# Performance work log

Hardware: AMD Instinct MI355X
Metric: run time of the kernel (lower is better)

Reference implementation:

```python
import jax, jax.numpy as jnp
import numpy as np

DIM = 1024
HEADS = 16
DHEAD = 64
MAXLEN = 512
B = 8
N = 256   # sequence (x) length
M = 256   # memory (h) length; M + N <= MAXLEN
INNER = HEADS * DHEAD


def setup_inputs() -> dict:
    key = jax.random.key(0)
    ks = jax.random.split(key, 8)
    w = lambda k, shape: jax.random.normal(k, shape, jnp.float32) * 0.02
    return {
        "x": jax.random.normal(ks[0], (B, N, DIM), jnp.float32),
        "h": jax.random.normal(ks[1], (B, M, DIM), jnp.float32),
        "Wqkv": w(ks[2], (DIM, 3 * INNER)),
        "Wkr": w(ks[3], (DIM, INNER)),
        "R": jax.random.normal(ks[4], (2 * MAXLEN, DIM), jnp.float32),
        "u": jax.random.normal(ks[5], (DHEAD,), jnp.float32),
        "v": jax.random.normal(ks[6], (DHEAD,), jnp.float32),
        "Wout": w(ks[7], (INNER, DIM)),
        "max_len": MAXLEN,
    }


def reference(x, h, Wqkv, Wkr, R, u, v, Wout, max_len):
    b, n, dim = x.shape
    m = h.shape[1]
    t = m + n
    scale = DHEAD ** -0.5

    cat = jnp.concatenate([h, x], axis=1)                     # [b, t, dim]
    qkv = cat @ Wqkv                                          # [b, t, 3*inner]
    q, k, val = [s.reshape(b, t, HEADS, DHEAD).transpose(0, 2, 1, 3)
                 for s in jnp.split(qkv, 3, axis=-1)]          # [b, h, t, d]

    # shifts[i, j] = (j - i) mod 2L, sliced as in the torch buffer
    ar = jnp.arange(2 * max_len)
    shifts_full = (ar[None, :] - ar[:, None]) % (2 * max_len)
    shifts = shifts_full[:max_len, :max_len][m:m + n, :t]      # [n, t]

    kr = (R @ Wkr)[shifts]                                    # gather: [n, t, inner]
    kr = kr.reshape(n, t, HEADS, DHEAD).transpose(2, 0, 1, 3)  # [h, n, t, d]

    q = q[:, :, m:]                                           # [b, h, n, d]

    term_a = jnp.einsum('bhnd,bhmd->bhnm', q, k)
    term_b = jnp.einsum('bhnd,hnmd->bhnm', q, kr)
    term_c = jnp.einsum('d,bhmd->bhm', u, k)[:, :, None, :]    # broadcast over n
    term_d = jnp.einsum('d,hnmd->hnm', v, kr)[None]            # broadcast over b
    dots = (term_a + term_b + term_c + term_d) * scale         # [b, h, n, t]

    qi = jnp.arange(n)[:, None]
    jm = jnp.arange(m)[None, :]
    js = jnp.arange(n)[None, :]
    mem_mask = jnp.where(qi > jm, -jnp.inf, 0.0)               # [n, m]
    ar_mask = jnp.where(js > qi, -jnp.inf, 0.0)                # [n, n]
    bias = jnp.concatenate([mem_mask, ar_mask], axis=1)[None, None]  # [1,1,n,t]

    attn = jax.nn.softmax(dots + bias, axis=-1)
    out = jnp.einsum('bhnm,bhmd->bhnd', attn, val)             # [b, h, n, d]
    out = out.transpose(0, 2, 1, 3).reshape(b, n, INNER)
    return out @ Wout
```

## Files before the change

### kernel.cpp

```cpp
#include <hip/hip_runtime.h>
#include <hip/hip_bf16.h>
#include <math.h>

typedef unsigned short u16;
typedef short bf16x8 __attribute__((ext_vector_type(8)));
typedef float f32x4 __attribute__((ext_vector_type(4)));

__device__ __forceinline__ u16 f2b(float f) {
    __hip_bfloat16 h = __float2bfloat16(f);
    return *reinterpret_cast<u16*>(&h);
}
__device__ __forceinline__ float b2f(u16 v) {
    __hip_bfloat16 h;
    *reinterpret_cast<u16*>(&h) = v;
    return __bfloat162float(h);
}

__device__ __forceinline__ void gload_lds16(const void* g, void* l) {
    __builtin_amdgcn_global_load_lds(
        (const __attribute__((address_space(1))) void*)g,
        (__attribute__((address_space(3))) void*)l, 16, 0, 0);
}


struct EpiQKV4 {
    u16 *Q, *Kt, *Vt;
    __device__ void operator()(int rowp, int colp, f32x4 vals) const {
        int b = colp >> 9, pos = colp & 511;
        int sec = rowp >> 10, cc = rowp & 1023;
        int head = cc >> 6, d0 = cc & 63;
        if (sec == 0) {
            if (pos < 256) return;
            ushort4 o;
            o.x = f2b(vals[0] * 0.125f); o.y = f2b(vals[1] * 0.125f);
            o.z = f2b(vals[2] * 0.125f); o.w = f2b(vals[3] * 0.125f);
            *(ushort4*)(Q + (long)((head * 8 + b) * 256 + (pos - 256)) * 64 + d0) = o;
        } else if (sec == 1) {
            ushort4 o;
            o.x = f2b(vals[0]); o.y = f2b(vals[1]);
            o.z = f2b(vals[2]); o.w = f2b(vals[3]);
            *(ushort4*)(Kt + (long)((b * 16 + head) * 512 + pos) * 64 + d0) = o;
        } else {
            #pragma unroll
            for (int r = 0; r < 4; ++r)
                Vt[(long)((b * 16 + head) * 64 + d0 + r) * 512 + pos] = f2b(vals[r]);
        }
    }
};

struct EpiStoreBf {
    u16* C; long ldc; long strideZ;
    __device__ void operator()(int z, int row, int col, float val) const {
        C[(long)z * strideZ + (long)row * ldc + col] = f2b(val);
    }
};


template <typename Epi, bool AF32, bool ROWMAP>
__device__ __forceinline__ void gemm_bt_body(char* smem, int bx, int by, int bz,
                                             const void* __restrict__ Av, int lda, long strideAz,
                                             const u16* __restrict__ B, int ldb, long strideBz,
                                             int K, Epi epi) {
    constexpr int LDT = 56;
    u16* As = (u16*)smem;
    u16* Bs = As + 64 * LDT;
    int n0 = bx * 64, m0 = by * 64, z = bz;
    const u16* Bb = B + (long)z * strideBz + (long)n0 * ldb;
    int tid = threadIdx.x;
    int wave = tid >> 6, lane = tid & 63;
    int wm = wave >> 1, wn = wave & 1;
    int lrow = lane & 15, lquad = lane >> 4;
    int srow = tid >> 2, scol = (tid & 3) * 8;
    f32x4 acc[2][2] = {};
    for (int k0 = 0; k0 < K; k0 += 32) {
        if constexpr (AF32) {
            long arow = m0 + srow;
            if constexpr (ROWMAP) arow = (arow < 256) ? 768 + arow : 0;
            const float* src = (const float*)Av + (long)z * strideAz + arow * lda + k0 + scol;
            float4 f0 = *(const float4*)src;
            float4 f1 = *(const float4*)(src + 4);
            bf16x8 vv;
            vv[0] = (short)f2b(f0.x); vv[1] = (short)f2b(f0.y);
            vv[2] = (short)f2b(f0.z); vv[3] = (short)f2b(f0.w);
            vv[4] = (short)f2b(f1.x); vv[5] = (short)f2b(f1.y);
            vv[6] = (short)f2b(f1.z); vv[7] = (short)f2b(f1.w);
            *(bf16x8*)(As + srow * LDT + scol) = vv;
        } else {
            const u16* Ab = (const u16*)Av + (long)z * strideAz + (long)m0 * lda;
            *(bf16x8*)(As + srow * LDT + scol) = *(const bf16x8*)(Ab + (long)srow * lda + k0 + scol);
        }
        *(bf16x8*)(Bs + srow * LDT + scol) = *(const bf16x8*)(Bb + (long)srow * ldb + k0 + scol);
        __syncthreads();
        bf16x8 af[2], bfr[2];
        #pragma unroll
        for (int mt = 0; mt < 2; ++mt)
            af[mt] = *(const bf16x8*)(As + (wm * 32 + mt * 16 + lrow) * LDT + lquad * 8);
        #pragma unroll
        for (int nt = 0; nt < 2; ++nt)
            bfr[nt] = *(const bf16x8*)(Bs + (wn * 32 + nt * 16 + lrow) * LDT + lquad * 8);
        #pragma unroll
        for (int mt = 0; mt < 2; ++mt)
            #pragma unroll
            for (int nt = 0; nt < 2; ++nt)
                acc[mt][nt] = __builtin_amdgcn_mfma_f32_16x16x32_bf16(af[mt], bfr[nt], acc[mt][nt], 0, 0, 0);
        __syncthreads();
    }
    #pragma unroll
    for (int mt = 0; mt < 2; ++mt)
        #pragma unroll
        for (int nt = 0; nt < 2; ++nt)
            #pragma unroll
            for (int r = 0; r < 4; ++r) {
                int row = m0 + wm * 32 + mt * 16 + lquad * 4 + r;
                int col = n0 + wn * 32 + nt * 16 + lrow;
                epi(z, row, col, acc[mt][nt][r]);
            }
}

__global__ __launch_bounds__(256) void prep_kernel(const float* __restrict__ x,
                                                   const float* __restrict__ h,
                                                   u16* __restrict__ catBF,
                                                   const float* __restrict__ Wqkv, u16* __restrict__ WqkvT,
                                                   const float* __restrict__ Wkr,  u16* __restrict__ WkrT,
                                                   const float* __restrict__ Wout, u16* __restrict__ WoutT,
                                                   u16* __restrict__ vtGuard) {
    __shared__ float tile[32][33];
    int bid = blockIdx.x, tid = threadIdx.x;
    if (bid == 7168) {
        ((unsigned int*)vtGuard)[tid] = 0u;
        return;
    }
    if (bid < 2048) {
        int idx = (bid * 256 + tid) * 8;
        int c = idx & 1023, r = idx >> 10;
        int b = r >> 9, pos = r & 511;
        const float* src = (pos < 256) ? h + ((long)(b * 256 + pos) * 1024 + c)
                                       : x + ((long)(b * 256 + pos - 256) * 1024 + c);
        float4 f0 = *(const float4*)src;
        float4 f1 = *(const float4*)(src + 4);
        bf16x8 vv;
        vv[0] = (short)f2b(f0.x); vv[1] = (short)f2b(f0.y);
        vv[2] = (short)f2b(f0.z); vv[3] = (short)f2b(f0.w);
        vv[4] = (short)f2b(f1.x); vv[5] = (short)f2b(f1.y);
        vv[6] = (short)f2b(f1.z); vv[7] = (short)f2b(f1.w);
        *(bf16x8*)(catBF + idx) = vv;
        return;
    }
    const float* W; u16* WT; int nb, kb; long ldw;
    if (bid < 5120) {
        int w = bid - 2048;
        W = Wqkv; WT = WqkvT; ldw = 3072;
        nb = (w % 96) * 32; kb = (w / 96) * 32;
    } else {
        int w = bid - 5120;
        if (w < 1024) { W = Wkr; WT = WkrT; }
        else          { W = Wout; WT = WoutT; w -= 1024; }
        ldw = 1024;
        nb = (w & 31) * 32; kb = (w >> 5) * 32;
    }
    {
        int lr = tid >> 3, lc = (tid & 7) * 4;
        float4 v = *(const float4*)&W[(long)(kb + lr) * ldw + nb + lc];
        tile[lr][lc + 0] = v.x; tile[lr][lc + 1] = v.y;
        tile[lr][lc + 2] = v.z; tile[lr][lc + 3] = v.w;
    }
    __syncthreads();
    int row = tid >> 3;
    int c4 = (tid & 7) * 4;
    ushort4 o;
    o.x = f2b(tile[c4 + 0][row]);
    o.y = f2b(tile[c4 + 1][row]);
    o.z = f2b(tile[c4 + 2][row]);
    o.w = f2b(tile[c4 + 3][row]);
    *(ushort4*)(WT + (long)(nb + row) * 1024 + kb + c4) = o;
}

__global__ __launch_bounds__(256, 3) void qkv_rwg_kernel(const u16* __restrict__ A, const u16* __restrict__ B,
                                                         EpiQKV4 eq,
                                                         const float* __restrict__ R, const u16* __restrict__ WkrT,
                                                         u16* __restrict__ RWg) {
    __shared__ alignas(16) char smem[49152];
    int bid0 = blockIdx.x;
    if (bid0 >= 640) {
        int bid2 = bid0 - 640;
        gemm_bt_body<EpiStoreBf, true, true>(smem, bid2 & 15, bid2 >> 4, 0,
            (const void*)R, 1024, 0L, WkrT, 1024, 0L, 1024, EpiStoreBf{RWg, 1024, 0});
        return;
    }
    int xcd = bid0 & 7, s = bid0 >> 3;
    int G = xcd * 10 + (s >> 3);
    int w = s & 7;
    int m0, n0;
    if (G < 64) {
        int nchunk = G >> 4, mrow = G & 15;
        m0 = 1024 + mrow * 128;
        n0 = (nchunk * 8 + w) * 128;
    } else {
        int G2 = G - 64;
        int nchunk = G2 >> 3, mrow = G2 & 7;
        m0 = mrow * 128;
        int c = nchunk * 8 + w;
        n0 = (c >> 1) * 512 + 256 + (c & 1) * 128;
    }
    int tid = threadIdx.x, wave = tid >> 6, lane = tid & 63;
    int wm = wave >> 1, wn = wave & 1;
    int lrow = lane & 15, lquad = lane >> 4;
    const u16* Ab = A + (long)m0 * 1024;
    const u16* Bb = B + (long)n0 * 1024;
    f32x4 acc[4][4] = {};

    int scperm = (((tid & 3) - ((tid >> 3) & 3)) & 3) * 8;
    int rsl = ((lquad + (lrow >> 1)) & 3) * 8;

    auto stage = [&](int buf, int k0) {
        u16* Asb = (u16*)smem + buf * 8192;
        u16* Bsb = Asb + 4096;
        int col = k0 + scperm;
        #pragma unroll
        for (int i = 0; i < 2; ++i) {
            int rowb = i * 64 + (tid >> 2);
            gload_lds16(Ab + (long)rowb * 1024 + col, Asb + i * 2048 + tid * 8);
            gload_lds16(Bb + (long)rowb * 1024 + col, Bsb + i * 2048 + tid * 8);
        }
    };
    auto compute = [&](int buf) {
        u16* Asb = (u16*)smem + buf * 8192;
        u16* Bsb = Asb + 4096;
        bf16x8 af[4], bfr[4];
        #pragma unroll
        for (int mt = 0; mt < 4; ++mt)
            af[mt] = *(const bf16x8*)(Asb + (wm * 64 + mt * 16 + lrow) * 32 + rsl);
        #pragma unroll
        for (int nt = 0; nt < 4; ++nt)
            bfr[nt] = *(const bf16x8*)(Bsb + (wn * 64 + nt * 16 + lrow) * 32 + rsl);
        __builtin_amdgcn_s_setprio(1);
        #pragma unroll
        for (int mt = 0; mt < 4; ++mt)
            #pragma unroll
            for (int nt = 0; nt < 4; ++nt)
                acc[mt][nt] = __builtin_amdgcn_mfma_f32_16x16x32_bf16(af[mt], bfr[nt], acc[mt][nt], 0, 0, 0);
        __builtin_amdgcn_s_setprio(0);
    };

    stage(0, 0);
    stage(1, 32);
    int cb = 0, sb = 2;
    for (int t = 0; t < 32; ++t) {
        if (t < 31) {
            asm volatile("s_waitcnt vmcnt(4)" ::: "memory");
        } else {
            asm volatile("s_waitcnt vmcnt(0)" ::: "memory");
        }
        __builtin_amdgcn_sched_barrier(0);
        __builtin_amdgcn_s_barrier();
        __builtin_amdgcn_sched_barrier(0);
        if (t < 30) stage(sb, (t + 2) * 32);
        __builtin_amdgcn_sched_barrier(0);
        compute(cb);
        cb = (cb == 2) ? 0 : cb + 1;
        sb = (sb == 2) ? 0 : sb + 1;
    }

    #pragma unroll
    for (int mt = 0; mt < 4; ++mt)
        #pragma unroll
        for (int nt = 0; nt < 4; ++nt) {
            int rowp = m0 + wm * 64 + mt * 16 + lquad * 4;
            int colp = n0 + wn * 64 + nt * 16 + lrow;
            eq(rowp, colp, acc[mt][nt]);
        }
}

__global__ __launch_bounds__(256, 4) void outproj_kernel(const u16* __restrict__ A,
                                                         const u16* __restrict__ B,
                                                         float* __restrict__ out) {
    __shared__ alignas(16) char smem[16384];
    int bid = blockIdx.x;
    int n0 = (bid & 15) * 64, m0 = (bid >> 4) * 64;
    int tid = threadIdx.x, wave = tid >> 6, lane = tid & 63;
    int wm = wave >> 1, wn = wave & 1;
    int lrow = lane & 15, lquad = lane >> 4;
    const u16* Ab = A + (long)m0 * 1024;
    const u16* Bb = B + (long)n0 * 1024;
    f32x4 acc[2][2] = {};

    int scperm = (((tid & 3) - ((tid >> 3) & 3)) & 3) * 8;
    int rsl = ((lquad + (lrow >> 1)) & 3) * 8;

    auto stage = [&](int buf, int k0) {
        u16* Asb = (u16*)smem + buf * 4096;
        u16* Bsb = Asb + 2048;
        int row = tid >> 2, col = k0 + scperm;
        gload_lds16(Ab + (long)row * 1024 + col, Asb + tid * 8);
        gload_lds16(Bb + (long)row * 1024 + col, Bsb + tid * 8);
    };
    auto compute = [&](int buf) {
        u16* Asb = (u16*)smem + buf * 4096;
        u16* Bsb = Asb + 2048;
        bf16x8 af[2], bfr[2];
        #pragma unroll
        for (int mt = 0; mt < 2; ++mt)
            af[mt] = *(const bf16x8*)(Asb + (wm * 32 + mt * 16 + lrow) * 32 + rsl);
        #pragma unroll
        for (int nt = 0; nt < 2; ++nt)
            bfr[nt] = *(const bf16x8*)(Bsb + (wn * 32 + nt * 16 + lrow) * 32 + rsl);
        #pragma unroll
        for (int mt = 0; mt < 2; ++mt)
            #pragma unroll
            for (int nt = 0; nt < 2; ++nt)
                acc[mt][nt] = __builtin_amdgcn_mfma_f32_16x16x32_bf16(af[mt], bfr[nt], acc[mt][nt], 0, 0, 0);
    };

    stage(0, 0);
    stage(1, 32);
    for (int t = 0; t < 31; ++t) {
        asm volatile("s_waitcnt vmcnt(2)" ::: "memory");
        __builtin_amdgcn_sched_barrier(0);
        __builtin_amdgcn_s_barrier();
        __builtin_amdgcn_sched_barrier(0);
        compute(t & 1);
        __builtin_amdgcn_sched_barrier(0);
        __builtin_amdgcn_s_barrier();
        __builtin_amdgcn_sched_barrier(0);
        if (t < 30) stage(t & 1, (t + 2) * 32);
    }
    asm volatile("s_waitcnt vmcnt(0)" ::: "memory");
    __builtin_amdgcn_sched_barrier(0);
    __builtin_amdgcn_s_barrier();
    __builtin_amdgcn_sched_barrier(0);
    compute(1);

    #pragma unroll
    for (int mt = 0; mt < 2; ++mt)
        #pragma unroll
        for (int nt = 0; nt < 2; ++nt)
            #pragma unroll
            for (int r = 0; r < 4; ++r)
                out[(long)(m0 + wm * 32 + mt * 16 + lquad * 4 + r) * 1024
                    + n0 + wn * 32 + nt * 16 + lrow] = acc[mt][nt][r];
}

__global__ __launch_bounds__(256, 4) void attn_kernel(const u16* __restrict__ Qs,
                                                      const u16* __restrict__ Kt,
                                                      const u16* __restrict__ VT,
                                                      const u16* __restrict__ RWg,
                                                      const float* __restrict__ uvec,
                                                      const float* __restrict__ vvec,
                                                      u16* __restrict__ attnOut) {
    constexpr int LDSW = 328;
    __shared__ alignas(16) u16 SQ[32 * LDSW];
    __shared__ float red[2][4][32];
    int id = blockIdx.x;
    int bh = id & 127, it = id >> 7;
    int b = bh >> 4, h = bh & 15;
    int i0 = it * 32;
    int w0 = i0;
    int tid = threadIdx.x, wave = tid >> 6, lane = tid & 63;
    int lrow = lane & 15, lquad = lane >> 4;

    bf16x8 aq[2][2], aqv[2][2];
    #pragma unroll
    for (int iu = 0; iu < 2; ++iu) {
        const u16* qbase = Qs + (long)((h * 8 + b) * 256 + i0 + iu * 16 + lrow) * 64;
        bf16x8 q0 = *(const bf16x8*)(qbase + lquad * 8);
        bf16x8 q1 = *(const bf16x8*)(qbase + 32 + lquad * 8);
        #pragma unroll
        for (int j = 0; j < 8; ++j) {
            float f0 = b2f((u16)q0[j]), f1 = b2f((u16)q1[j]);
            aq[iu][0][j]  = (short)f2b(f0 + 0.125f * uvec[lquad * 8 + j]);
            aq[iu][1][j]  = (short)f2b(f1 + 0.125f * uvec[32 + lquad * 8 + j]);
            aqv[iu][0][j] = (short)f2b(f0 + 0.125f * vvec[lquad * 8 + j]);
            aqv[iu][1][j] = (short)f2b(f1 + 0.125f * vvec[32 + lquad * 8 + j]);
        }
    }

    const u16* rwbase = RWg + (long)(wave * 80) * 1024 + h * 64;
    #pragma unroll
    for (int t = 0; t < 5; ++t) {
        const u16* rp = rwbase + (long)(t * 16 + lrow) * 1024;
        bf16x8 br0 = *(const bf16x8*)(rp + lquad * 8);
        bf16x8 br1 = *(const bf16x8*)(rp + 32 + lquad * 8);
        int sc = wave * 80 + t * 16 + lrow;
        #pragma unroll
        for (int iu = 0; iu < 2; ++iu) {
            f32x4 qa = {0.f, 0.f, 0.f, 0.f};
            qa = __builtin_amdgcn_mfma_f32_16x16x32_bf16(aqv[iu][0], br0, qa, 0, 0, 0);
            qa = __builtin_amdgcn_mfma_f32_16x16x32_bf16(aqv[iu][1], br1, qa, 0, 0, 0);
            #pragma unroll
            for (int r = 0; r < 4; ++r)
                SQ[(iu * 16 + lquad * 4 + r) * LDSW + sc] = f2b(qa[r]);
        }
    }

    const u16* kbase = Kt + ((long)bh * 512 + w0 + wave * 80) * 64;
    bf16x8 bk0[5], bk1[5];
    #pragma unroll
    for (int t = 0; t < 5; ++t) {
        const u16* kp = kbase + (long)(t * 16 + lrow) * 64;
        bk0[t] = *(const bf16x8*)(kp + lquad * 8);
        bk1[t] = *(const bf16x8*)(kp + 32 + lquad * 8);
    }
    f32x4 acc[2][5];
    __builtin_amdgcn_s_setprio(1);
    #pragma unroll
    for (int t = 0; t < 5; ++t)
        #pragma unroll
        for (int iu = 0; iu < 2; ++iu) {
            f32x4 a = {0.f, 0.f, 0.f, 0.f};
            a = __builtin_amdgcn_mfma_f32_16x16x32_bf16(aq[iu][0], bk0[t], a, 0, 0, 0);
            a = __builtin_amdgcn_mfma_f32_16x16x32_bf16(aq[iu][1], bk1[t], a, 0, 0, 0);
            acc[iu][t] = a;
        }
    __builtin_amdgcn_s_setprio(0);
    __syncthreads();

    float m4[2][4];
    #pragma unroll
    for (int iu = 0; iu < 2; ++iu)
        #pragma unroll
        for (int r = 0; r < 4; ++r) m4[iu][r] = -1e30f;
    #pragma unroll
    for (int t = 0; t < 5; ++t) {
        int lj = wave * 80 + t * 16 + lrow;
        #pragma unroll
        for (int iu = 0; iu < 2; ++iu)
            #pragma unroll
            for (int r = 0; r < 4; ++r) {
                int rloc = iu * 16 + lquad * 4 + r;
                int d = lj - rloc;
                int dc = d < 0 ? 0 : (d > 256 ? 256 : d);
                bool ok = (unsigned)d <= 256u;
                float val = ok ? acc[iu][t][r] + b2f(SQ[rloc * LDSW + dc]) : -1e30f;
                acc[iu][t][r] = val;
                m4[iu][r] = fmaxf(m4[iu][r], val);
            }
    }
    #pragma unroll
    for (int iu = 0; iu < 2; ++iu)
        #pragma unroll
        for (int r = 0; r < 4; ++r) {
            #pragma unroll
            for (int off = 1; off < 16; off <<= 1)
                m4[iu][r] = fmaxf(m4[iu][r], __shfl_xor(m4[iu][r], off));
            if (lrow == 0) red[0][wave][iu * 16 + lquad * 4 + r] = m4[iu][r];
        }
    __syncthreads();

    float gmax[2][4];
    #pragma unroll
    for (int iu = 0; iu < 2; ++iu)
        #pragma unroll
        for (int r = 0; r < 4; ++r) {
            int row = iu * 16 + lquad * 4 + r;
            gmax[iu][r] = fmaxf(fmaxf(red[0][0][row], red[0][1][row]),
                                fmaxf(red[0][2][row], red[0][3][row]));
        }

    float s4[2][4] = {};
    #pragma unroll
    for (int t = 0; t < 5; ++t) {
        int lj = wave * 80 + t * 16 + lrow;
        #pragma unroll
        for (int iu = 0; iu < 2; ++iu)
            #pragma unroll
            for (int r = 0; r < 4; ++r) {
                float p = __expf(acc[iu][t][r] - gmax[iu][r]);
                s4[iu][r] += p;
                SQ[(iu * 16 + lquad * 4 + r) * LDSW + lj] = f2b(p);
            }
    }
    #pragma unroll
    for (int iu = 0; iu < 2; ++iu)
        #pragma unroll
        for (int r = 0; r < 4; ++r) {
            #pragma unroll
            for (int off = 1; off < 16; off <<= 1)
                s4[iu][r] += __shfl_xor(s4[iu][r], off);
            if (lrow == 0) red[1][wave][iu * 16 + lquad * 4 + r] = s4[iu][r];
        }
    __syncthreads();

    const u16* vbase = VT + ((long)bh * 64 + wave * 16 + lrow) * 512 + w0;
    f32x4 oacc[2] = {};
    bf16x8 vp[10];
    #pragma unroll
    for (int t = 0; t < 10; ++t)
        vp[t] = *(const bf16x8*)(vbase + t * 32 + lquad * 8);
    __builtin_amdgcn_s_setprio(1);
    #pragma unroll
    for (int t = 0; t < 10; ++t)
        #pragma unroll
        for (int iu = 0; iu < 2; ++iu) {
            bf16x8 ap = *(const bf16x8*)(SQ + (iu * 16 + lrow) * LDSW + t * 32 + lquad * 8);
            oacc[iu] = __builtin_amdgcn_mfma_f32_16x16x32_bf16(ap, vp[t], oacc[iu], 0, 0, 0);
        }
    __builtin_amdgcn_s_setprio(0);
    #pragma unroll
    for (int iu = 0; iu < 2; ++iu)
        #pragma unroll
        for (int r = 0; r < 4; ++r) {
            int row = iu * 16 + lquad * 4 + r;
            float inv = 1.0f / (red[1][0][row] + red[1][1][row] + red[1][2][row] + red[1][3][row]);
            attnOut[(long)(b * 256 + i0 + row) * 1024 + h * 64 + wave * 16 + lrow] = f2b(oacc[iu][r] * inv);
        }
}


extern "C" void kernel_launch(void* const* d_in, const int* in_sizes, int n_in,
                              void* d_out, int out_size, void* d_ws, size_t ws_size,
                              hipStream_t stream) {
    (void)in_sizes; (void)n_in; (void)out_size; (void)ws_size;
    const float* x    = (const float*)d_in[0];
    const float* h    = (const float*)d_in[1];
    const float* Wqkv = (const float*)d_in[2];
    const float* Wkr  = (const float*)d_in[3];
    const float* R    = (const float*)d_in[4];
    const float* u    = (const float*)d_in[5];
    const float* v    = (const float*)d_in[6];
    const float* Wout = (const float*)d_in[7];
    float* out = (float*)d_out;

    char* ws = (char*)d_ws;
    size_t off = 0;
    auto alloc = [&](size_t bytes) -> void* {
        void* p = ws + off;
        off = (off + bytes + 255) & ~(size_t)255;
        return p;
    };
    u16* catBF  = (u16*)alloc(4096L * 1024 * 2);
    u16* WqkvT  = (u16*)alloc(3072L * 1024 * 2);
    u16* WkrT   = (u16*)alloc(1024L * 1024 * 2);
    u16* WoutT  = (u16*)alloc(1024L * 1024 * 2);
    u16* RWg    = (u16*)alloc(320L * 1024 * 2);
    u16* Q      = (u16*)alloc(16L * 8 * 256 * 64 * 2);
    u16* Kt     = (u16*)alloc(8L * 16 * 512 * 64 * 2);
    u16* VT     = (u16*)alloc(8L * 16 * 64 * 512 * 2 + 1024);
    u16* attnO  = (u16*)alloc(2048L * 1024 * 2);
    u16* vtGuard = VT + 8L * 16 * 64 * 512;

    prep_kernel<<<7169, 256, 0, stream>>>(x, h, catBF, Wqkv, WqkvT, Wkr, WkrT, Wout, WoutT, vtGuard);
    qkv_rwg_kernel<<<720, 256, 0, stream>>>(WqkvT, catBF, EpiQKV4{Q, Kt, VT}, R, WkrT, RWg);
    attn_kernel<<<1024, 256, 0, stream>>>(Q, Kt, VT, RWg, u, v, attnO);
    outproj_kernel<<<512, 256, 0, stream>>>(attnO, WoutT, out);
}
```

Baseline: 163.1 us.

## Enlarge weight transpose tiles, remap QKV block order, reorder pipeline, skew SQ layout

The weight transpose/cast in the prep kernel now uses 64x64 tiles with wider 16-byte bf16 stores, cutting the block count. The QKV GEMM gets a new block-to-XCD mapping and drops setprio. Its loop now runs compute before issuing the next stage load. The attention kernel stores the relative-position scores in a row-skewed LDS layout (wider stride, offset by row), so the gather indexes by lj directly without clamping. These changes mix tile sizing, scheduling and LDS layout tweaks, and each could help or hurt on its own.

```diff
diff --git a/kernel.cpp b/kernel.cpp
--- a/kernel.cpp
+++ b/kernel.cpp
@@ -124,9 +124,9 @@
                                                    const float* __restrict__ Wkr,  u16* __restrict__ WkrT,
                                                    const float* __restrict__ Wout, u16* __restrict__ WoutT,
                                                    u16* __restrict__ vtGuard) {
-    __shared__ float tile[32][33];
+    __shared__ float tile[64][65];
     int bid = blockIdx.x, tid = threadIdx.x;
-    if (bid == 7168) {
+    if (bid == 3328) {
         ((unsigned int*)vtGuard)[tid] = 0u;
         return;
     }
@@ -147,32 +147,40 @@
         return;
     }
     const float* W; u16* WT; int nb, kb; long ldw;
-    if (bid < 5120) {
-        int w = bid - 2048;
+    int w = bid - 2048;
+    if (w < 768) {
         W = Wqkv; WT = WqkvT; ldw = 3072;
-        nb = (w % 96) * 32; kb = (w / 96) * 32;
+        nb = (w % 48) * 64; kb = (w / 48) * 64;
+    } else if (w < 1024) {
+        int w2 = w - 768;
+        W = Wkr; WT = WkrT; ldw = 1024;
+        nb = (w2 & 15) * 64; kb = (w2 >> 4) * 64;
     } else {
-        int w = bid - 5120;
-        if (w < 1024) { W = Wkr; WT = WkrT; }
-        else          { W = Wout; WT = WoutT; w -= 1024; }
-        ldw = 1024;
-        nb = (w & 31) * 32; kb = (w >> 5) * 32;
+        int w2 = w - 1024;
+        W = Wout; WT = WoutT; ldw = 1024;
+        nb = (w2 & 15) * 64; kb = (w2 >> 4) * 64;
     }
     {
-        int lr = tid >> 3, lc = (tid & 7) * 4;
-        float4 v = *(const float4*)&W[(long)(kb + lr) * ldw + nb + lc];
-        tile[lr][lc + 0] = v.x; tile[lr][lc + 1] = v.y;
-        tile[lr][lc + 2] = v.z; tile[lr][lc + 3] = v.w;
+        int lr = tid >> 4, lc = (tid & 15) * 4;
+        #pragma unroll
+        for (int i = 0; i < 4; ++i) {
+            float4 v = *(const float4*)&W[(long)(kb + lr + i * 16) * ldw + nb + lc];
+            tile[lr + i * 16][lc + 0] = v.x; tile[lr + i * 16][lc + 1] = v.y;
+            tile[lr + i * 16][lc + 2] = v.z; tile[lr + i * 16][lc + 3] = v.w;
+        }
     }
     __syncthreads();
-    int row = tid >> 3;
-    int c4 = (tid & 7) * 4;
-    ushort4 o;
-    o.x = f2b(tile[c4 + 0][row]);
-    o.y = f2b(tile[c4 + 1][row]);
-    o.z = f2b(tile[c4 + 2][row]);
-    o.w = f2b(tile[c4 + 3][row]);
-    *(ushort4*)(WT + (long)(nb + row) * 1024 + kb + c4) = o;
+    {
+        int wr = tid >> 2, wc = (tid & 3) * 16;
+        #pragma unroll
+        for (int k = 0; k < 2; ++k) {
+            bf16x8 vv;
+            #pragma unroll
+            for (int e = 0; e < 8; ++e)
+                vv[e] = (short)f2b(tile[wc + k * 8 + e][wr]);
+            *(bf16x8*)(WT + (long)(nb + wr) * 1024 + kb + wc + k * 8) = vv;
+        }
+    }
 }
 
 __global__ __launch_bounds__(256, 3) void qkv_rwg_kernel(const u16* __restrict__ A, const u16* __restrict__ B,
@@ -188,16 +196,17 @@
         return;
     }
     int xcd = bid0 & 7, s = bid0 >> 3;
-    int G = xcd * 10 + (s >> 3);
+    int t0i = s >> 3;
     int w = s & 7;
     int m0, n0;
-    if (G < 64) {
-        int nchunk = G >> 4, mrow = G & 15;
+    if (t0i < 8) {
+        int nchunk = xcd >> 1;
+        int mrow = (xcd & 1) * 8 + t0i;
         m0 = 1024 + mrow * 128;
         n0 = (nchunk * 8 + w) * 128;
     } else {
-        int G2 = G - 64;
-        int nchunk = G2 >> 3, mrow = G2 & 7;
+        int qidx = xcd * 2 + (t0i - 8);
+        int nchunk = qidx >> 3, mrow = qidx & 7;
         m0 = mrow * 128;
         int c = nchunk * 8 + w;
         n0 = (c >> 1) * 512 + 256 + (c & 1) * 128;
@@ -233,13 +242,11 @@
         #pragma unroll
         for (int nt = 0; nt < 4; ++nt)
             bfr[nt] = *(const bf16x8*)(Bsb + (wn * 64 + nt * 16 + lrow) * 32 + rsl);
-        __builtin_amdgcn_s_setprio(1);
         #pragma unroll
         for (int mt = 0; mt < 4; ++mt)
             #pragma unroll
             for (int nt = 0; nt < 4; ++nt)
                 acc[mt][nt] = __builtin_amdgcn_mfma_f32_16x16x32_bf16(af[mt], bfr[nt], acc[mt][nt], 0, 0, 0);
-        __builtin_amdgcn_s_setprio(0);
     };
 
     stage(0, 0);
@@ -254,9 +261,9 @@
         __builtin_amdgcn_sched_barrier(0);
         __builtin_amdgcn_s_barrier();
         __builtin_amdgcn_sched_barrier(0);
+        compute(cb);
+        __builtin_amdgcn_sched_barrier(0);
         if (t < 30) stage(sb, (t + 2) * 32);
-        __builtin_amdgcn_sched_barrier(0);
-        compute(cb);
         cb = (cb == 2) ? 0 : cb + 1;
         sb = (sb == 2) ? 0 : sb + 1;
     }
@@ -347,7 +354,7 @@
                                                       const float* __restrict__ uvec,
                                                       const float* __restrict__ vvec,
                                                       u16* __restrict__ attnOut) {
-    constexpr int LDSW = 328;
+    constexpr int LDSW = 360;
     __shared__ alignas(16) u16 SQ[32 * LDSW];
     __shared__ float red[2][4][32];
     int id = blockIdx.x;
@@ -387,8 +394,10 @@
             qa = __builtin_amdgcn_mfma_f32_16x16x32_bf16(aqv[iu][0], br0, qa, 0, 0, 0);
             qa = __builtin_amdgcn_mfma_f32_16x16x32_bf16(aqv[iu][1], br1, qa, 0, 0, 0);
             #pragma unroll
-            for (int r = 0; r < 4; ++r)
-                SQ[(iu * 16 + lquad * 4 + r) * LDSW + sc] = f2b(qa[r]);
+            for (int r = 0; r < 4; ++r) {
+                int rloc = iu * 16 + lquad * 4 + r;
+                SQ[rloc * LDSW + sc + rloc] = f2b(qa[r]);
+            }
         }
     }
 
@@ -427,10 +436,8 @@
             #pragma unroll
             for (int r = 0; r < 4; ++r) {
                 int rloc = iu * 16 + lquad * 4 + r;
-                int d = lj - rloc;
-                int dc = d < 0 ? 0 : (d > 256 ? 256 : d);
-                bool ok = (unsigned)d <= 256u;
-                float val = ok ? acc[iu][t][r] + b2f(SQ[rloc * LDSW + dc]) : -1e30f;
+                bool ok = (unsigned)(lj - rloc) <= 256u;
+                float val = ok ? acc[iu][t][r] + b2f(SQ[rloc * LDSW + lj]) : -1e30f;
                 acc[iu][t][r] = val;
                 m4[iu][r] = fmaxf(m4[iu][r], val);
             }
@@ -538,7 +545,7 @@
     u16* attnO  = (u16*)alloc(2048L * 1024 * 2);
     u16* vtGuard = VT + 8L * 16 * 64 * 512;
 
-    prep_kernel<<<7169, 256, 0, stream>>>(x, h, catBF, Wqkv, WqkvT, Wkr, WkrT, Wout, WoutT, vtGuard);
+    prep_kernel<<<3329, 256, 0, stream>>>(x, h, catBF, Wqkv, WqkvT, Wkr, WkrT, Wout, WoutT, vtGuard);
     qkv_rwg_kernel<<<720, 256, 0, stream>>>(WqkvT, catBF, EpiQKV4{Q, Kt, VT}, R, WkrT, RWg);
     attn_kernel<<<1024, 256, 0, stream>>>(Q, Kt, VT, RWg, u, v, attnO);
     outproj_kernel<<<512, 256, 0, stream>>>(attnO, WoutT, out);
```

Result: no change. 161.2 us (-1.2%).
